# Kernel tuning notes

Hardware: AMD Instinct MI355X
Metric: run time of the kernel (lower is better)

## Reference

```python
import jax, jax.numpy as jnp
import numpy as np

H = 128      # num_hidden
C = 384      # num_in
K = 32       # neighbors
N = 10000    # nodes
SCALE = 30.0
EPS = 1e-5

def _gelu(x):
    return jax.nn.gelu(x, approximate=False)  # torch GELU default is exact erf

def _ln(x, g, b):
    m = jnp.mean(x, axis=-1, keepdims=True)
    v = jnp.mean((x - m) ** 2, axis=-1, keepdims=True)
    return (x - m) * jax.lax.rsqrt(v + EPS) * g + b

def setup_inputs() -> dict:
    key = jax.random.key(0)
    ks = jax.random.split(key, 12)
    s = lambda fan_in: 1.0 / np.sqrt(fan_in)
    # weights stored [in, out] (transposed vs torch nn.Linear)
    return {
        "h_V": jax.random.normal(ks[0], (N, H), jnp.float32),
        "h_E": jax.random.normal(ks[1], (N, K, C), jnp.float32),
        "mask_V": jnp.ones((N,), jnp.float32),
        "mask_attend": jnp.ones((N, K), jnp.float32),
        "W1_w": jax.random.uniform(ks[2], (H + C, H), jnp.float32, -s(H + C), s(H + C)),
        "W1_b": jnp.zeros((H,), jnp.float32),
        "W2_w": jax.random.uniform(ks[3], (H, H), jnp.float32, -s(H), s(H)),
        "W2_b": jnp.zeros((H,), jnp.float32),
        "W3_w": jax.random.uniform(ks[4], (H, H), jnp.float32, -s(H), s(H)),
        "W3_b": jnp.zeros((H,), jnp.float32),
        "ln1_g": jnp.ones((H,), jnp.float32),
        "ln1_b": jnp.zeros((H,), jnp.float32),
        "Win_w": jax.random.uniform(ks[5], (H, 4 * H), jnp.float32, -s(H), s(H)),
        "Win_b": jnp.zeros((4 * H,), jnp.float32),
        "Wout_w": jax.random.uniform(ks[6], (4 * H, H), jnp.float32, -s(4 * H), s(4 * H)),
        "Wout_b": jnp.zeros((H,), jnp.float32),
        "ln2_g": jnp.ones((H,), jnp.float32),
        "ln2_b": jnp.zeros((H,), jnp.float32),
    }

def reference(h_V, h_E, mask_V, mask_attend,
              W1_w, W1_b, W2_w, W2_b, W3_w, W3_b,
              ln1_g, ln1_b, Win_w, Win_b, Wout_w, Wout_b, ln2_g, ln2_b):
    # expand node features along neighbor axis and concat with edge features
    h_V_expand = jnp.broadcast_to(h_V[:, None, :], (h_V.shape[0], h_E.shape[1], h_V.shape[1]))
    h_EV = jnp.concatenate([h_V_expand, h_E], axis=-1)          # [N, K, H+C]
    # per-edge 3-layer MLP message
    h = _gelu(h_EV @ W1_w + W1_b)                               # [N, K, H]
    h = _gelu(h @ W2_w + W2_b)
    h_message = h @ W3_w + W3_b
    h_message = mask_attend[..., None] * h_message
    dh = jnp.sum(h_message, axis=-2) / SCALE                    # [N, H]
    h_V = _ln(h_V + dh, ln1_g, ln1_b)
    # position-wise FFN
    dh = _gelu(h_V @ Win_w + Win_b) @ Wout_w + Wout_b
    h_V = _ln(h_V + dh, ln2_g, ln2_b)
    h_V = mask_V[:, None] * h_V
    return h_V
```

## Files before the change

kernel.cpp:

```cpp
#include <hip/hip_runtime.h>
#include <hip/hip_bf16.h>

#define NH 128
#define NC 384
#define NK 32

typedef __attribute__((ext_vector_type(8))) short short8v;
typedef __attribute__((ext_vector_type(4))) float f32x4;

#define MFMA16(a, b, c) __builtin_amdgcn_mfma_f32_16x16x32_bf16((a), (b), (c), 0, 0, 0)

__device__ __forceinline__ ushort f2bf(float x) {
  __hip_bfloat16 h = __float2bfloat16(x);
  ushort u;
  __builtin_memcpy(&u, &h, 2);
  return u;
}

__device__ __forceinline__ short8v ld8(const ushort* p) {
  return *reinterpret_cast<const short8v*>(p);
}
__device__ __forceinline__ void st8(ushort* p, short8v v) {
  *reinterpret_cast<short8v*>(p) = v;
}

__device__ __forceinline__ short8v pack8(float4 a, float4 b) {
  short8v v;
  v[0] = (short)f2bf(a.x); v[1] = (short)f2bf(a.y);
  v[2] = (short)f2bf(a.z); v[3] = (short)f2bf(a.w);
  v[4] = (short)f2bf(b.x); v[5] = (short)f2bf(b.y);
  v[6] = (short)f2bf(b.z); v[7] = (short)f2bf(b.w);
  return v;
}

__device__ __forceinline__ float gelu_f(float x) {
  float x2 = x * x;
  float m = __builtin_fmaf(0.07135481283f, x2, 1.595769122f);
  float e = __expf(-x * m);
  return x * __builtin_amdgcn_rcpf(1.0f + e);
}

__global__ __launch_bounds__(256) void pack_w(
    const float* __restrict__ W1, const float* __restrict__ W2,
    const float* __restrict__ W3, const float* __restrict__ Win,
    const float* __restrict__ Wout, ushort* __restrict__ ws) {
  int id = blockIdx.x * 256 + threadIdx.x;
  if (id < 65536) {
    int t = id, k = t >> 7, c = t & 127;
    ws[(((k >> 3) << 7) + c) * 8 + (k & 7)] = f2bf(W1[t]);
  } else if (id < 81920) {
    int t = id - 65536, k = t >> 7, c = t & 127;
    ws[65536 + (((k >> 3) << 7) + c) * 8 + (k & 7)] = f2bf(W2[t]);
  } else if (id < 98304) {
    int t = id - 81920, k = t >> 7, c = t & 127;
    ws[81920 + (((k >> 3) << 7) + c) * 8 + (k & 7)] = f2bf(W3[t]);
  } else if (id < 163840) {
    int t = id - 98304, k = t >> 9, c = t & 511;
    ws[98304 + (((k >> 3) << 9) + c) * 8 + (k & 7)] = f2bf(Win[t]);
  } else {
    int t = id - 163840, k = t >> 7, c = t & 127;
    ws[163840 + (((k >> 3) << 7) + c) * 8 + (k & 7)] = f2bf(Wout[t]);
  }
}

__global__ __launch_bounds__(512, 4) void msg_kernel(
    const float* __restrict__ hV, const float* __restrict__ hE,
    const float* __restrict__ mAtt, const ushort* __restrict__ wsu,
    const float* __restrict__ b1, const float* __restrict__ b2,
    const float* __restrict__ b3, const float* __restrict__ g1,
    const float* __restrict__ be1, float* __restrict__ hmidf,
    ushort* __restrict__ hmidb, int N) {
  const ushort* W1p = wsu;
  const ushort* W2p = wsu + 65536;
  const ushort* W3p = wsu + 81920;

  __shared__ ushort sEb[2][64 * 128];
  __shared__ ushort sHV[2 * NH];
  __shared__ ushort sH1[64 * 128];
  __shared__ float  sDh[2 * NH];
  __shared__ float  sRed[16];
  ushort* sH2 = sEb[0];

  const int tid = threadIdx.x;
  const int w = tid >> 6, lane = tid & 63;
  const int g = lane >> 4, lr = lane & 15;
  const int n0 = blockIdx.x * 2;

  const int row = tid >> 3, cb = tid & 7;
  const int node = row >> 5, e = row & 31;
  const bool valid = (n0 + node) < N;
  const float* src = hE + (valid ? ((size_t)(n0 + node) * NK + e) * NC : 0);
  float4 L[3][2][2];
#pragma unroll
  for (int q = 0; q < 3; ++q)
#pragma unroll
    for (int h = 0; h < 2; ++h) {
      const float4* p = reinterpret_cast<const float4*>(src + q * 128 + h * 64 + cb * 8);
      L[q][h][0] = p[0];
      L[q][h][1] = p[1];
    }

  if (tid < 32) {
    const int nd = tid >> 4, c8 = tid & 15;
    short8v v = {0, 0, 0, 0, 0, 0, 0, 0};
    if (n0 + nd < N) {
      const float4* p = reinterpret_cast<const float4*>(hV + (size_t)(n0 + nd) * NH + c8 * 8);
      v = pack8(p[0], p[1]);
    }
    st8(sHV + nd * NH + c8 * 8, v);
  }

  const int rsw = row & 15;
#pragma unroll
  for (int h = 0; h < 2; ++h) {
    short8v v = valid ? pack8(L[0][h][0], L[0][h][1]) : (short8v){0, 0, 0, 0, 0, 0, 0, 0};
    st8(&sEb[0][row * 128 + (((cb + 8 * h) ^ rsw) << 3)], v);
  }
  __syncthreads();

  const int colbase = (w << 4) + lr;
  f32x4 acc[4];
#pragma unroll
  for (int rt = 0; rt < 4; ++rt) acc[rt] = (f32x4){0.f, 0.f, 0.f, 0.f};

#pragma unroll
  for (int kt = 0; kt < 4; ++kt) {
    short8v b = ld8(W1p + ((kt * 4 + g) * 128 + colbase) * 8);
    short8v a0 = ld8(sHV + kt * 32 + g * 8);
    short8v a1 = ld8(sHV + NH + kt * 32 + g * 8);
    acc[0] = MFMA16(a0, b, acc[0]);
    acc[1] = MFMA16(a0, b, acc[1]);
    acc[2] = MFMA16(a1, b, acc[2]);
    acc[3] = MFMA16(a1, b, acc[3]);
  }
#pragma unroll
  for (int j = 0; j < 4; ++j) {
    short8v b = ld8(W1p + (((4 + j) * 4 + g) * 128 + colbase) * 8);
    const int kcg = j * 4 + g;
#pragma unroll
    for (int rt = 0; rt < 4; ++rt) {
      const int r2 = rt * 16 + lr;
      short8v a = ld8(&sEb[0][r2 * 128 + ((kcg ^ (r2 & 15)) << 3)]);
      acc[rt] = MFMA16(a, b, acc[rt]);
    }
  }
#pragma unroll
  for (int h = 0; h < 2; ++h) {
    short8v v = valid ? pack8(L[1][h][0], L[1][h][1]) : (short8v){0, 0, 0, 0, 0, 0, 0, 0};
    st8(&sEb[1][row * 128 + (((cb + 8 * h) ^ rsw) << 3)], v);
  }
  __syncthreads();

#pragma unroll
  for (int j = 0; j < 4; ++j) {
    short8v b = ld8(W1p + (((8 + j) * 4 + g) * 128 + colbase) * 8);
    const int kcg = j * 4 + g;
#pragma unroll
    for (int rt = 0; rt < 4; ++rt) {
      const int r2 = rt * 16 + lr;
      short8v a = ld8(&sEb[1][r2 * 128 + ((kcg ^ (r2 & 15)) << 3)]);
      acc[rt] = MFMA16(a, b, acc[rt]);
    }
  }
#pragma unroll
  for (int h = 0; h < 2; ++h) {
    short8v v = valid ? pack8(L[2][h][0], L[2][h][1]) : (short8v){0, 0, 0, 0, 0, 0, 0, 0};
    st8(&sEb[0][row * 128 + (((cb + 8 * h) ^ rsw) << 3)], v);
  }
  __syncthreads();

#pragma unroll
  for (int j = 0; j < 4; ++j) {
    short8v b = ld8(W1p + (((12 + j) * 4 + g) * 128 + colbase) * 8);
    const int kcg = j * 4 + g;
#pragma unroll
    for (int rt = 0; rt < 4; ++rt) {
      const int r2 = rt * 16 + lr;
      short8v a = ld8(&sEb[0][r2 * 128 + ((kcg ^ (r2 & 15)) << 3)]);
      acc[rt] = MFMA16(a, b, acc[rt]);
    }
  }
  {
    const float bias = b1[colbase];
#pragma unroll
    for (int rt = 0; rt < 4; ++rt) {
#pragma unroll
      for (int i = 0; i < 4; ++i) {
        const int rr = rt * 16 + g * 4 + i;
        const float vv = gelu_f(acc[rt][i] + bias);
        sH1[rr * 128 + ((((colbase >> 3) ^ (rr & 15)) << 3) | (colbase & 7))] = f2bf(vv);
      }
    }
  }
  __syncthreads();

#pragma unroll
  for (int rt = 0; rt < 4; ++rt) acc[rt] = (f32x4){0.f, 0.f, 0.f, 0.f};
#pragma unroll
  for (int kt = 0; kt < 4; ++kt) {
    short8v b = ld8(W2p + ((kt * 4 + g) * 128 + colbase) * 8);
    const int kcg = kt * 4 + g;
#pragma unroll
    for (int rt = 0; rt < 4; ++rt) {
      const int r2 = rt * 16 + lr;
      short8v a = ld8(&sH1[r2 * 128 + ((kcg ^ (r2 & 15)) << 3)]);
      acc[rt] = MFMA16(a, b, acc[rt]);
    }
  }
  {
    const float bias = b2[colbase];
#pragma unroll
    for (int rt = 0; rt < 4; ++rt) {
#pragma unroll
      for (int i = 0; i < 4; ++i) {
        const int rr = rt * 16 + g * 4 + i;
        const float vv = gelu_f(acc[rt][i] + bias);
        sH2[rr * 128 + ((((colbase >> 3) ^ (rr & 15)) << 3) | (colbase & 7))] = f2bf(vv);
      }
    }
  }
  __syncthreads();

#pragma unroll
  for (int rt = 0; rt < 4; ++rt) acc[rt] = (f32x4){0.f, 0.f, 0.f, 0.f};
#pragma unroll
  for (int kt = 0; kt < 4; ++kt) {
    short8v b = ld8(W3p + ((kt * 4 + g) * 128 + colbase) * 8);
    const int kcg = kt * 4 + g;
#pragma unroll
    for (int rt = 0; rt < 4; ++rt) {
      const int r2 = rt * 16 + lr;
      short8v a = ld8(&sH2[r2 * 128 + ((kcg ^ (r2 & 15)) << 3)]);
      acc[rt] = MFMA16(a, b, acc[rt]);
    }
  }
  {
    const float bias = b3[colbase];
    float ns0 = 0.f, ns1 = 0.f;
#pragma unroll
    for (int rt = 0; rt < 4; ++rt) {
      const int nd = rt >> 1;
      float s = 0.f;
#pragma unroll
      for (int i = 0; i < 4; ++i) {
        const int e2 = (rt & 1) * 16 + g * 4 + i;
        const float m = (n0 + nd < N) ? mAtt[(size_t)(n0 + nd) * NK + e2] : 0.f;
        s += (acc[rt][i] + bias) * m;
      }
      s += __shfl_xor(s, 16, 64);
      s += __shfl_xor(s, 32, 64);
      if (rt < 2) ns0 += s; else ns1 += s;
    }
    if (g == 0) { sDh[colbase] = ns0; sDh[NH + colbase] = ns1; }
  }
  __syncthreads();

  float x_ln = 0.f;
  if (tid < 256) {
    const int nd = tid >> 7, i = tid & 127;
    const int gn = n0 + nd;
    if (gn < N) x_ln = hV[(size_t)gn * NH + i] + sDh[nd * NH + i] * (1.f / 30.f);
    float s = x_ln, qv = x_ln * x_ln;
#pragma unroll
    for (int d = 1; d < 64; d <<= 1) {
      s += __shfl_xor(s, d, 64);
      qv += __shfl_xor(qv, d, 64);
    }
    if (lane == 0) { sRed[w * 2] = s; sRed[w * 2 + 1] = qv; }
  }
  __syncthreads();
  if (tid < 256) {
    const int nd = tid >> 7, i = tid & 127;
    const int gn = n0 + nd;
    if (gn < N) {
      const int wb = nd * 2;
      const float s = sRed[wb * 2] + sRed[wb * 2 + 2];
      const float qv = sRed[wb * 2 + 1] + sRed[wb * 2 + 3];
      const float mean = s * (1.f / 128.f);
      const float var = qv * (1.f / 128.f) - mean * mean;
      const float y = (x_ln - mean) * rsqrtf(var + 1e-5f) * g1[i] + be1[i];
      hmidf[(size_t)gn * NH + i] = y;
      hmidb[(size_t)gn * NH + i] = f2bf(y);
    }
  }
}

__global__ __launch_bounds__(256, 4) void ffn_kernel(
    const ushort* __restrict__ wsu, const float* __restrict__ binf,
    const float* __restrict__ boutf, const float* __restrict__ g2,
    const float* __restrict__ be2, const float* __restrict__ maskV,
    const float* __restrict__ hmidf, const ushort* __restrict__ hmidb,
    float* __restrict__ out, int N) {
  const ushort* Winp = wsu + 98304;
  const ushort* Woutp = wsu + 163840;

  __shared__ ushort sX[16 * 128];
  __shared__ ushort sHf[16 * 512];
  __shared__ float  sY[16 * 132];

  const int tid = threadIdx.x;
  const int w = tid >> 6, lane = tid & 63;
  const int g = lane >> 4, lr = lane & 15;
  const int n0 = blockIdx.x * 16;

  {
    const int rr = tid >> 4, c8 = tid & 15;
    const int n = n0 + rr;
    short8v v = {0, 0, 0, 0, 0, 0, 0, 0};
    if (n < N) v = ld8(hmidb + (size_t)n * NH + c8 * 8);
    st8(sX + rr * 128 + ((c8 ^ (rr & 15)) << 3), v);
  }
  __syncthreads();

#pragma unroll
  for (int ct8 = 0; ct8 < 8; ++ct8) {
    const int col = (w * 8 + ct8) * 16 + lr;
    f32x4 a0acc = (f32x4){0.f, 0.f, 0.f, 0.f};
#pragma unroll
    for (int kt = 0; kt < 4; ++kt) {
      short8v b = ld8(Winp + ((kt * 4 + g) * 512 + col) * 8);
      const int kcg = kt * 4 + g;
      const int r0 = lr;
      short8v a0 = ld8(sX + r0 * 128 + ((kcg ^ (r0 & 15)) << 3));
      a0acc = MFMA16(a0, b, a0acc);
    }
    const float bi = binf[col];
#pragma unroll
    for (int i = 0; i < 4; ++i) {
      const int rr = g * 4 + i;
      const float v0 = gelu_f(a0acc[i] + bi);
      sHf[rr * 512 + ((((col >> 3) ^ (rr & 15)) << 3) | (col & 7))] = f2bf(v0);
    }
  }
  __syncthreads();

  f32x4 o0 = (f32x4){0.f, 0.f, 0.f, 0.f}, o1 = o0;
#pragma unroll
  for (int kt = 0; kt < 16; ++kt) {
    const int kcg = kt * 4 + g;
    const int c0 = (2 * w) * 16 + lr, c1 = (2 * w + 1) * 16 + lr;
    short8v b0 = ld8(Woutp + (kcg * 128 + c0) * 8);
    short8v b1 = ld8(Woutp + (kcg * 128 + c1) * 8);
    const int r0 = lr;
    short8v a0 = ld8(sHf + r0 * 512 + ((kcg ^ (r0 & 15)) << 3));
    o0 = MFMA16(a0, b0, o0);
    o1 = MFMA16(a0, b1, o1);
  }
#pragma unroll
  for (int ct = 0; ct < 2; ++ct) {
    const int col = (2 * w + ct) * 16 + lr;
    const float bo = boutf[col];
    const f32x4 oo = ct ? o1 : o0;
#pragma unroll
    for (int i = 0; i < 4; ++i) {
      const int rr = g * 4 + i;
      const int n = n0 + rr;
      const float resid = (n < N) ? hmidf[(size_t)n * NH + col] : 0.f;
      sY[rr * 132 + col] = oo[i] + bo + resid;
    }
  }
  __syncthreads();

  {
    const int rr = tid >> 4, qq = tid & 15;
    const int n = n0 + rr;
    float vals[8];
    float s = 0.f, qs = 0.f;
    const float* yr = sY + rr * 132 + qq * 8;
#pragma unroll
    for (int j = 0; j < 8; ++j) { float x = yr[j]; vals[j] = x; s += x; qs += x * x; }
    s += __shfl_xor(s, 1, 64);  qs += __shfl_xor(qs, 1, 64);
    s += __shfl_xor(s, 2, 64);  qs += __shfl_xor(qs, 2, 64);
    s += __shfl_xor(s, 4, 64);  qs += __shfl_xor(qs, 4, 64);
    s += __shfl_xor(s, 8, 64);  qs += __shfl_xor(qs, 8, 64);
    const float mean = s * (1.f / 128.f);
    const float var = qs * (1.f / 128.f) - mean * mean;
    const float rs = rsqrtf(var + 1e-5f);
    if (n < N) {
      const float mv = maskV[n];
#pragma unroll
      for (int j = 0; j < 8; ++j) {
        const int col = qq * 8 + j;
        out[(size_t)n * NH + col] = ((vals[j] - mean) * rs * g2[col] + be2[col]) * mv;
      }
    }
  }
}

extern "C" void kernel_launch(void* const* d_in, const int* in_sizes, int n_in,
                              void* d_out, int out_size, void* d_ws, size_t ws_size,
                              hipStream_t stream) {
  const float* hV   = (const float*)d_in[0];
  const float* hE   = (const float*)d_in[1];
  const float* mV   = (const float*)d_in[2];
  const float* mAtt = (const float*)d_in[3];
  const float* W1   = (const float*)d_in[4];
  const float* b1   = (const float*)d_in[5];
  const float* W2   = (const float*)d_in[6];
  const float* b2   = (const float*)d_in[7];
  const float* W3   = (const float*)d_in[8];
  const float* b3   = (const float*)d_in[9];
  const float* g1   = (const float*)d_in[10];
  const float* be1  = (const float*)d_in[11];
  const float* Win  = (const float*)d_in[12];
  const float* binf = (const float*)d_in[13];
  const float* Wout = (const float*)d_in[14];
  const float* bout = (const float*)d_in[15];
  const float* g2   = (const float*)d_in[16];
  const float* be2  = (const float*)d_in[17];

  const int N = in_sizes[0] / NH;

  ushort* wsu = (ushort*)d_ws;
  float*  hmidf = (float*)((char*)d_ws + 458752);
  ushort* hmidb = (ushort*)((char*)d_ws + 458752 + (size_t)N * NH * 4);
  float*  outp = (float*)d_out;

  pack_w<<<896, 256, 0, stream>>>(W1, W2, W3, Win, Wout, wsu);
  msg_kernel<<<(N + 1) / 2, 512, 0, stream>>>(hV, hE, mAtt, wsu, b1, b2, b3,
                                              g1, be1, hmidf, hmidb, N);
  ffn_kernel<<<(N + 15) / 16, 256, 0, stream>>>(wsu, binf, bout, g2, be2, mV,
                                                hmidf, hmidb, outp, N);
  (void)n_in; (void)out_size; (void)ws_size;
}
```

Before: 183.0 us.

## Fuse message and FFN kernels into persistent kernel with software-pipelined edge loads

Merges the message MLP kernel and the FFN kernel into one persistent kernel with a fixed grid of 512 blocks. Each block loops over node pairs and prefetches the next pair's edge features, node features and masks into registers and double-buffered LDS while the current pair computes. The post-LN1 intermediate stays in shared memory (up to 20 rows), and the FFN plus LN2 run at the end on those rows, so the global hmid round trip and the second launch go away. The trade-off is fewer blocks (512 instead of 5000), more synchronisation per iteration and higher LDS/register pressure, which may cut occupancy and weaken latency hiding.

```diff
diff --git a/kernel.cpp b/kernel.cpp
--- a/kernel.cpp
+++ b/kernel.cpp
@@ -63,325 +63,341 @@
   }
 }
 
-__global__ __launch_bounds__(512, 4) void msg_kernel(
+__global__ __launch_bounds__(512, 4) void msg_ffn(
     const float* __restrict__ hV, const float* __restrict__ hE,
-    const float* __restrict__ mAtt, const ushort* __restrict__ wsu,
+    const float* __restrict__ maskV, const float* __restrict__ mAtt,
+    const ushort* __restrict__ wsu,
     const float* __restrict__ b1, const float* __restrict__ b2,
     const float* __restrict__ b3, const float* __restrict__ g1,
-    const float* __restrict__ be1, float* __restrict__ hmidf,
-    ushort* __restrict__ hmidb, int N) {
+    const float* __restrict__ be1, const float* __restrict__ binf,
+    const float* __restrict__ bout, const float* __restrict__ g2,
+    const float* __restrict__ be2, float* __restrict__ out, int N) {
   const ushort* W1p = wsu;
   const ushort* W2p = wsu + 65536;
   const ushort* W3p = wsu + 81920;
-
-  __shared__ ushort sEb[2][64 * 128];
-  __shared__ ushort sHV[2 * NH];
-  __shared__ ushort sH1[64 * 128];
-  __shared__ float  sDh[2 * NH];
+  const ushort* Winp = wsu + 98304;
+  const ushort* Woutp = wsu + 163840;
+
+  __shared__ ushort sEb[2][8192];
+  __shared__ float  sHmidF[20 * 132];
+  __shared__ ushort sHV[2][256];
+  __shared__ float  sHVf[2][256];
+  __shared__ float  sMA[2][64];
+  __shared__ float  sDh[256];
   __shared__ float  sRed[16];
-  ushort* sH2 = sEb[0];
 
   const int tid = threadIdx.x;
   const int w = tid >> 6, lane = tid & 63;
   const int g = lane >> 4, lr = lane & 15;
-  const int n0 = blockIdx.x * 2;
-
-  const int row = tid >> 3, cb = tid & 7;
-  const int node = row >> 5, e = row & 31;
-  const bool valid = (n0 + node) < N;
-  const float* src = hE + (valid ? ((size_t)(n0 + node) * NK + e) * NC : 0);
-  float4 L[3][2][2];
-#pragma unroll
-  for (int q = 0; q < 3; ++q)
+  const int colbase = (w << 4) + lr;
+
+  const int pairsTotal = (N + 1) >> 1;
+  const int bId = blockIdx.x;
+  const int stride = gridDim.x;
+  const int T = (bId < pairsTotal) ? ((pairsTotal - bId + stride - 1) / stride) : 0;
+
+  const int srow = tid >> 3, scb = tid & 7;
+  const int snode = srow >> 5, sedge = srow & 31;
+  const int rsw = srow & 15;
+
+  float4 Lb0[2][2], Lb1[2][2], Lc2[2][2];
+  float4 hvreg = (float4){0.f, 0.f, 0.f, 0.f};
+  float  mareg = 0.f;
+  bool   zhold = true;
+
+  auto hEbase = [&](int p) -> const float* {
+    int n = 2 * p + snode;
+    int nc = n < N ? n : 0;
+    return hE + ((size_t)nc * NK + sedge) * NC + scb * 8;
+  };
+  auto loadCh = [&](const float* bp, int q, float4 L[2][2]) {
+    const float4* p0 = reinterpret_cast<const float4*>(bp + q * 128);
+    const float4* p1 = reinterpret_cast<const float4*>(bp + q * 128 + 64);
+    L[0][0] = p0[0]; L[0][1] = p0[1];
+    L[1][0] = p1[0]; L[1][1] = p1[1];
+  };
+  auto writeCh = [&](ushort* buf, float4 L[2][2], bool zz) {
 #pragma unroll
     for (int h = 0; h < 2; ++h) {
-      const float4* p = reinterpret_cast<const float4*>(src + q * 128 + h * 64 + cb * 8);
-      L[q][h][0] = p[0];
-      L[q][h][1] = p[1];
-    }
-
-  if (tid < 32) {
-    const int nd = tid >> 4, c8 = tid & 15;
-    short8v v = {0, 0, 0, 0, 0, 0, 0, 0};
-    if (n0 + nd < N) {
-      const float4* p = reinterpret_cast<const float4*>(hV + (size_t)(n0 + nd) * NH + c8 * 8);
-      v = pack8(p[0], p[1]);
-    }
-    st8(sHV + nd * NH + c8 * 8, v);
-  }
-
-  const int rsw = row & 15;
-#pragma unroll
-  for (int h = 0; h < 2; ++h) {
-    short8v v = valid ? pack8(L[0][h][0], L[0][h][1]) : (short8v){0, 0, 0, 0, 0, 0, 0, 0};
-    st8(&sEb[0][row * 128 + (((cb + 8 * h) ^ rsw) << 3)], v);
-  }
-  __syncthreads();
-
-  const int colbase = (w << 4) + lr;
-  f32x4 acc[4];
-#pragma unroll
-  for (int rt = 0; rt < 4; ++rt) acc[rt] = (f32x4){0.f, 0.f, 0.f, 0.f};
-
-#pragma unroll
-  for (int kt = 0; kt < 4; ++kt) {
-    short8v b = ld8(W1p + ((kt * 4 + g) * 128 + colbase) * 8);
-    short8v a0 = ld8(sHV + kt * 32 + g * 8);
-    short8v a1 = ld8(sHV + NH + kt * 32 + g * 8);
-    acc[0] = MFMA16(a0, b, acc[0]);
-    acc[1] = MFMA16(a0, b, acc[1]);
-    acc[2] = MFMA16(a1, b, acc[2]);
-    acc[3] = MFMA16(a1, b, acc[3]);
-  }
-#pragma unroll
-  for (int j = 0; j < 4; ++j) {
-    short8v b = ld8(W1p + (((4 + j) * 4 + g) * 128 + colbase) * 8);
-    const int kcg = j * 4 + g;
-#pragma unroll
-    for (int rt = 0; rt < 4; ++rt) {
-      const int r2 = rt * 16 + lr;
-      short8v a = ld8(&sEb[0][r2 * 128 + ((kcg ^ (r2 & 15)) << 3)]);
-      acc[rt] = MFMA16(a, b, acc[rt]);
-    }
-  }
-#pragma unroll
-  for (int h = 0; h < 2; ++h) {
-    short8v v = valid ? pack8(L[1][h][0], L[1][h][1]) : (short8v){0, 0, 0, 0, 0, 0, 0, 0};
-    st8(&sEb[1][row * 128 + (((cb + 8 * h) ^ rsw) << 3)], v);
-  }
-  __syncthreads();
-
-#pragma unroll
-  for (int j = 0; j < 4; ++j) {
-    short8v b = ld8(W1p + (((8 + j) * 4 + g) * 128 + colbase) * 8);
-    const int kcg = j * 4 + g;
-#pragma unroll
-    for (int rt = 0; rt < 4; ++rt) {
-      const int r2 = rt * 16 + lr;
-      short8v a = ld8(&sEb[1][r2 * 128 + ((kcg ^ (r2 & 15)) << 3)]);
-      acc[rt] = MFMA16(a, b, acc[rt]);
-    }
-  }
-#pragma unroll
-  for (int h = 0; h < 2; ++h) {
-    short8v v = valid ? pack8(L[2][h][0], L[2][h][1]) : (short8v){0, 0, 0, 0, 0, 0, 0, 0};
-    st8(&sEb[0][row * 128 + (((cb + 8 * h) ^ rsw) << 3)], v);
-  }
-  __syncthreads();
-
-#pragma unroll
-  for (int j = 0; j < 4; ++j) {
-    short8v b = ld8(W1p + (((12 + j) * 4 + g) * 128 + colbase) * 8);
-    const int kcg = j * 4 + g;
-#pragma unroll
-    for (int rt = 0; rt < 4; ++rt) {
-      const int r2 = rt * 16 + lr;
-      short8v a = ld8(&sEb[0][r2 * 128 + ((kcg ^ (r2 & 15)) << 3)]);
-      acc[rt] = MFMA16(a, b, acc[rt]);
-    }
-  }
-  {
-    const float bias = b1[colbase];
-#pragma unroll
-    for (int rt = 0; rt < 4; ++rt) {
+      short8v v = zz ? (short8v){0, 0, 0, 0, 0, 0, 0, 0} : pack8(L[h][0], L[h][1]);
+      st8(buf + srow * 128 + (((scb + 8 * h) ^ rsw) << 3), v);
+    }
+  };
+  auto loadHVMA = [&](int p) {
+    if (tid < 64) {
+      int nd = tid >> 5, c4 = tid & 31;
+      int n = 2 * p + nd;
+      int nc = n < N ? n : 0;
+      hvreg = *reinterpret_cast<const float4*>(hV + (size_t)nc * NH + c4 * 4);
+      if (n >= N) hvreg = (float4){0.f, 0.f, 0.f, 0.f};
+      mareg = (n < N) ? mAtt[(size_t)(2 * p) * NK + tid] : 0.f;
+    }
+  };
+  auto storeHVMA = [&](int par) {
+    if (tid < 64) {
+      int nd = tid >> 5, c4 = tid & 31;
+      *reinterpret_cast<float4*>(&sHVf[par][nd * 128 + c4 * 4]) = hvreg;
+      ushort4 hb;
+      hb.x = f2bf(hvreg.x); hb.y = f2bf(hvreg.y);
+      hb.z = f2bf(hvreg.z); hb.w = f2bf(hvreg.w);
+      *reinterpret_cast<ushort4*>(&sHV[par][nd * 128 + c4 * 4]) = hb;
+      sMA[par][tid] = mareg;
+    }
+  };
+  auto mfmaChunk = [&](const ushort* buf, int ktBase, f32x4 acc[4]) {
+#pragma unroll
+    for (int j = 0; j < 4; ++j) {
+      short8v bfr = ld8(W1p + (((ktBase + j) * 4 + g) * 128 + colbase) * 8);
+      const int kcg = j * 4 + g;
+#pragma unroll
+      for (int rt = 0; rt < 4; ++rt) {
+        const int row = rt * 16 + lr;
+        short8v a = ld8(buf + row * 128 + ((kcg ^ (row & 15)) << 3));
+        acc[rt] = MFMA16(a, bfr, acc[rt]);
+      }
+    }
+  };
+  auto mfma128 = [&](const ushort* Wp, const ushort* buf, f32x4 acc[4]) {
+#pragma unroll
+    for (int kt = 0; kt < 4; ++kt) {
+      short8v bfr = ld8(Wp + ((kt * 4 + g) * 128 + colbase) * 8);
+      const int kcg = kt * 4 + g;
+#pragma unroll
+      for (int rt = 0; rt < 4; ++rt) {
+        const int row = rt * 16 + lr;
+        short8v a = ld8(buf + row * 128 + ((kcg ^ (row & 15)) << 3));
+        acc[rt] = MFMA16(a, bfr, acc[rt]);
+      }
+    }
+  };
+  auto epiStore = [&](ushort* buf, f32x4 acc[4], const float* bias) {
+    const float bs = bias[colbase];
+#pragma unroll
+    for (int rt = 0; rt < 4; ++rt)
 #pragma unroll
       for (int i = 0; i < 4; ++i) {
         const int rr = rt * 16 + g * 4 + i;
-        const float vv = gelu_f(acc[rt][i] + bias);
-        sH1[rr * 128 + ((((colbase >> 3) ^ (rr & 15)) << 3) | (colbase & 7))] = f2bf(vv);
-      }
-    }
+        buf[rr * 128 + ((((colbase >> 3) ^ (rr & 15)) << 3) | (colbase & 7))] =
+            f2bf(gelu_f(acc[rt][i] + bs));
+      }
+  };
+
+  if (T > 0) {
+    const float* bp = hEbase(bId);
+    const bool z0 = (2 * bId + snode) >= N;
+    loadCh(bp, 0, Lb0);
+    loadCh(bp, 1, Lb1);
+    loadCh(bp, 2, Lc2);
+    loadHVMA(bId);
+    writeCh(sEb[0], Lb0, z0);
+    writeCh(sEb[1], Lb1, z0);
+    zhold = z0;
+    storeHVMA(0);
+    __syncthreads();
   }
-  __syncthreads();
-
-#pragma unroll
-  for (int rt = 0; rt < 4; ++rt) acc[rt] = (f32x4){0.f, 0.f, 0.f, 0.f};
-#pragma unroll
-  for (int kt = 0; kt < 4; ++kt) {
-    short8v b = ld8(W2p + ((kt * 4 + g) * 128 + colbase) * 8);
-    const int kcg = kt * 4 + g;
-#pragma unroll
-    for (int rt = 0; rt < 4; ++rt) {
-      const int r2 = rt * 16 + lr;
-      short8v a = ld8(&sH1[r2 * 128 + ((kcg ^ (r2 & 15)) << 3)]);
-      acc[rt] = MFMA16(a, b, acc[rt]);
-    }
-  }
-  {
-    const float bias = b2[colbase];
-#pragma unroll
-    for (int rt = 0; rt < 4; ++rt) {
-#pragma unroll
-      for (int i = 0; i < 4; ++i) {
-        const int rr = rt * 16 + g * 4 + i;
-        const float vv = gelu_f(acc[rt][i] + bias);
-        sH2[rr * 128 + ((((colbase >> 3) ^ (rr & 15)) << 3) | (colbase & 7))] = f2bf(vv);
-      }
-    }
-  }
-  __syncthreads();
-
-#pragma unroll
-  for (int rt = 0; rt < 4; ++rt) acc[rt] = (f32x4){0.f, 0.f, 0.f, 0.f};
-#pragma unroll
-  for (int kt = 0; kt < 4; ++kt) {
-    short8v b = ld8(W3p + ((kt * 4 + g) * 128 + colbase) * 8);
-    const int kcg = kt * 4 + g;
-#pragma unroll
-    for (int rt = 0; rt < 4; ++rt) {
-      const int r2 = rt * 16 + lr;
-      short8v a = ld8(&sH2[r2 * 128 + ((kcg ^ (r2 & 15)) << 3)]);
-      acc[rt] = MFMA16(a, b, acc[rt]);
-    }
-  }
-  {
-    const float bias = b3[colbase];
-    float ns0 = 0.f, ns1 = 0.f;
-#pragma unroll
-    for (int rt = 0; rt < 4; ++rt) {
-      const int nd = rt >> 1;
-      float s = 0.f;
-#pragma unroll
-      for (int i = 0; i < 4; ++i) {
-        const int e2 = (rt & 1) * 16 + g * 4 + i;
-        const float m = (n0 + nd < N) ? mAtt[(size_t)(n0 + nd) * NK + e2] : 0.f;
-        s += (acc[rt][i] + bias) * m;
-      }
-      s += __shfl_xor(s, 16, 64);
-      s += __shfl_xor(s, 32, 64);
-      if (rt < 2) ns0 += s; else ns1 += s;
-    }
-    if (g == 0) { sDh[colbase] = ns0; sDh[NH + colbase] = ns1; }
-  }
-  __syncthreads();
-
-  float x_ln = 0.f;
-  if (tid < 256) {
-    const int nd = tid >> 7, i = tid & 127;
-    const int gn = n0 + nd;
-    if (gn < N) x_ln = hV[(size_t)gn * NH + i] + sDh[nd * NH + i] * (1.f / 30.f);
-    float s = x_ln, qv = x_ln * x_ln;
-#pragma unroll
-    for (int d = 1; d < 64; d <<= 1) {
-      s += __shfl_xor(s, d, 64);
-      qv += __shfl_xor(qv, d, 64);
-    }
-    if (lane == 0) { sRed[w * 2] = s; sRed[w * 2 + 1] = qv; }
-  }
-  __syncthreads();
-  if (tid < 256) {
-    const int nd = tid >> 7, i = tid & 127;
-    const int gn = n0 + nd;
-    if (gn < N) {
+
+  for (int t = 0; t < T; ++t) {
+    const int par = t & 1, nxt = par ^ 1;
+    ushort* bufX = sEb[par];
+    ushort* bufY = sEb[nxt];
+
+    const int pn = bId + (t + 1) * stride;
+    const int pc = pn < pairsTotal ? pn : 0;
+    const bool zb = (2 * pc + snode) >= N;
+    const float* bp = hEbase(pc);
+    loadCh(bp, 0, Lb0);
+    loadCh(bp, 1, Lb1);
+    loadHVMA(pc);
+
+    f32x4 acc[4];
+#pragma unroll
+    for (int rt = 0; rt < 4; ++rt) acc[rt] = (f32x4){0.f, 0.f, 0.f, 0.f};
+#pragma unroll
+    for (int kt = 0; kt < 4; ++kt) {
+      short8v bfr = ld8(W1p + ((kt * 4 + g) * 128 + colbase) * 8);
+      short8v a0 = ld8(&sHV[par][kt * 32 + g * 8]);
+      short8v a1 = ld8(&sHV[par][128 + kt * 32 + g * 8]);
+      acc[0] = MFMA16(a0, bfr, acc[0]);
+      acc[1] = MFMA16(a0, bfr, acc[1]);
+      acc[2] = MFMA16(a1, bfr, acc[2]);
+      acc[3] = MFMA16(a1, bfr, acc[3]);
+    }
+    mfmaChunk(bufX, 4, acc);
+    __syncthreads();
+    writeCh(bufX, Lc2, zhold);
+    loadCh(bp, 2, Lc2);
+    zhold = zb;
+    mfmaChunk(bufY, 8, acc);
+    __syncthreads();
+    mfmaChunk(bufX, 12, acc);
+    __syncthreads();
+    epiStore(bufY, acc, b1);
+    __syncthreads();
+
+    f32x4 acc2[4];
+#pragma unroll
+    for (int rt = 0; rt < 4; ++rt) acc2[rt] = (f32x4){0.f, 0.f, 0.f, 0.f};
+    mfma128(W2p, bufY, acc2);
+    epiStore(bufX, acc2, b2);
+    __syncthreads();
+
+    f32x4 acc3[4];
+#pragma unroll
+    for (int rt = 0; rt < 4; ++rt) acc3[rt] = (f32x4){0.f, 0.f, 0.f, 0.f};
+    mfma128(W3p, bufX, acc3);
+    writeCh(bufY, Lb0, zb);
+    {
+      const float bias = b3[colbase];
+      float ns0 = 0.f, ns1 = 0.f;
+#pragma unroll
+      for (int rt = 0; rt < 4; ++rt) {
+        float s = 0.f;
+#pragma unroll
+        for (int i = 0; i < 4; ++i) {
+          const int e2 = (rt & 1) * 16 + g * 4 + i;
+          const int nd = rt >> 1;
+          s += (acc3[rt][i] + bias) * sMA[par][nd * 32 + e2];
+        }
+        s += __shfl_xor(s, 16, 64);
+        s += __shfl_xor(s, 32, 64);
+        if (rt < 2) ns0 += s; else ns1 += s;
+      }
+      if (g == 0) { sDh[colbase] = ns0; sDh[128 + colbase] = ns1; }
+    }
+    __syncthreads();
+
+    float x_ln = 0.f;
+    if (tid < 256) {
+      const int nd = tid >> 7, i = tid & 127;
+      x_ln = sHVf[par][nd * 128 + i] + sDh[nd * 128 + i] * (1.f / 30.f);
+      float s = x_ln, qv = x_ln * x_ln;
+#pragma unroll
+      for (int d = 1; d < 64; d <<= 1) {
+        s += __shfl_xor(s, d, 64);
+        qv += __shfl_xor(qv, d, 64);
+      }
+      if (lane == 0) { sRed[w * 2] = s; sRed[w * 2 + 1] = qv; }
+    }
+    writeCh(bufX, Lb1, zb);
+    storeHVMA(nxt);
+    __syncthreads();
+    if (tid < 256) {
+      const int nd = tid >> 7, i = tid & 127;
       const int wb = nd * 2;
       const float s = sRed[wb * 2] + sRed[wb * 2 + 2];
       const float qv = sRed[wb * 2 + 1] + sRed[wb * 2 + 3];
       const float mean = s * (1.f / 128.f);
       const float var = qv * (1.f / 128.f) - mean * mean;
       const float y = (x_ln - mean) * rsqrtf(var + 1e-5f) * g1[i] + be1[i];
-      hmidf[(size_t)gn * NH + i] = y;
-      hmidb[(size_t)gn * NH + i] = f2bf(y);
-    }
+      sHmidF[(2 * t + nd) * 132 + i] = y;
+    }
+    __syncthreads();
   }
-}
-
-__global__ __launch_bounds__(256, 4) void ffn_kernel(
-    const ushort* __restrict__ wsu, const float* __restrict__ binf,
-    const float* __restrict__ boutf, const float* __restrict__ g2,
-    const float* __restrict__ be2, const float* __restrict__ maskV,
-    const float* __restrict__ hmidf, const ushort* __restrict__ hmidb,
-    float* __restrict__ out, int N) {
-  const ushort* Winp = wsu + 98304;
-  const ushort* Woutp = wsu + 163840;
-
-  __shared__ ushort sX[16 * 128];
-  __shared__ ushort sHf[16 * 512];
-  __shared__ float  sY[16 * 132];
-
-  const int tid = threadIdx.x;
-  const int w = tid >> 6, lane = tid & 63;
-  const int g = lane >> 4, lr = lane & 15;
-  const int n0 = blockIdx.x * 16;
-
-  {
-    const int rr = tid >> 4, c8 = tid & 15;
-    const int n = n0 + rr;
-    short8v v = {0, 0, 0, 0, 0, 0, 0, 0};
-    if (n < N) v = ld8(hmidb + (size_t)n * NH + c8 * 8);
-    st8(sX + rr * 128 + ((c8 ^ (rr & 15)) << 3), v);
-  }
-  __syncthreads();
-
-#pragma unroll
-  for (int ct8 = 0; ct8 < 8; ++ct8) {
-    const int col = (w * 8 + ct8) * 16 + lr;
-    f32x4 a0acc = (f32x4){0.f, 0.f, 0.f, 0.f};
+
+  if (T > 0) {
+    const int R = 2 * T;
+    ushort* sHf = &sEb[0][0];
+    float*  sYF = reinterpret_cast<float*>(
+        reinterpret_cast<char*>(&sEb[0][0]) + 20480);
+
+    f32x4 accI[4][2];
+#pragma unroll
+    for (int ct = 0; ct < 4; ++ct)
+#pragma unroll
+      for (int rt = 0; rt < 2; ++rt) accI[ct][rt] = (f32x4){0.f, 0.f, 0.f, 0.f};
 #pragma unroll
     for (int kt = 0; kt < 4; ++kt) {
-      short8v b = ld8(Winp + ((kt * 4 + g) * 512 + col) * 8);
+      short8v afr[2];
+#pragma unroll
+      for (int rt = 0; rt < 2; ++rt) {
+        const int row = rt * 16 + lr;
+        if (row < R) {
+          const float4* ap =
+              reinterpret_cast<const float4*>(&sHmidF[row * 132 + kt * 32 + g * 8]);
+          afr[rt] = pack8(ap[0], ap[1]);
+        } else {
+          afr[rt] = (short8v){0, 0, 0, 0, 0, 0, 0, 0};
+        }
+      }
+#pragma unroll
+      for (int ct = 0; ct < 4; ++ct) {
+        const int col = (w << 6) + ct * 16 + lr;
+        short8v bfr = ld8(Winp + ((kt * 4 + g) * 512 + col) * 8);
+        accI[ct][0] = MFMA16(afr[0], bfr, accI[ct][0]);
+        accI[ct][1] = MFMA16(afr[1], bfr, accI[ct][1]);
+      }
+    }
+    __syncthreads();
+#pragma unroll
+    for (int ct = 0; ct < 4; ++ct) {
+      const int col = (w << 6) + ct * 16 + lr;
+      const float bi = binf[col];
+      const int c8 = col >> 3;
+#pragma unroll
+      for (int rt = 0; rt < 2; ++rt)
+#pragma unroll
+        for (int i = 0; i < 4; ++i) {
+          const int row = rt * 16 + g * 4 + i;
+          if (row < R)
+            sHf[row * 512 + (((c8 & 48) | ((c8 ^ row) & 15)) << 3) + (col & 7)] =
+                f2bf(gelu_f(accI[ct][rt][i] + bi));
+        }
+    }
+    __syncthreads();
+
+    f32x4 accO[2];
+    accO[0] = (f32x4){0.f, 0.f, 0.f, 0.f};
+    accO[1] = accO[0];
+#pragma unroll
+    for (int kt = 0; kt < 16; ++kt) {
       const int kcg = kt * 4 + g;
-      const int r0 = lr;
-      short8v a0 = ld8(sX + r0 * 128 + ((kcg ^ (r0 & 15)) << 3));
-      a0acc = MFMA16(a0, b, a0acc);
-    }
-    const float bi = binf[col];
-#pragma unroll
-    for (int i = 0; i < 4; ++i) {
-      const int rr = g * 4 + i;
-      const float v0 = gelu_f(a0acc[i] + bi);
-      sHf[rr * 512 + ((((col >> 3) ^ (rr & 15)) << 3) | (col & 7))] = f2bf(v0);
-    }
-  }
-  __syncthreads();
-
-  f32x4 o0 = (f32x4){0.f, 0.f, 0.f, 0.f}, o1 = o0;
-#pragma unroll
-  for (int kt = 0; kt < 16; ++kt) {
-    const int kcg = kt * 4 + g;
-    const int c0 = (2 * w) * 16 + lr, c1 = (2 * w + 1) * 16 + lr;
-    short8v b0 = ld8(Woutp + (kcg * 128 + c0) * 8);
-    short8v b1 = ld8(Woutp + (kcg * 128 + c1) * 8);
-    const int r0 = lr;
-    short8v a0 = ld8(sHf + r0 * 512 + ((kcg ^ (r0 & 15)) << 3));
-    o0 = MFMA16(a0, b0, o0);
-    o1 = MFMA16(a0, b1, o1);
-  }
-#pragma unroll
-  for (int ct = 0; ct < 2; ++ct) {
-    const int col = (2 * w + ct) * 16 + lr;
-    const float bo = boutf[col];
-    const f32x4 oo = ct ? o1 : o0;
-#pragma unroll
-    for (int i = 0; i < 4; ++i) {
-      const int rr = g * 4 + i;
-      const int n = n0 + rr;
-      const float resid = (n < N) ? hmidf[(size_t)n * NH + col] : 0.f;
-      sY[rr * 132 + col] = oo[i] + bo + resid;
-    }
-  }
-  __syncthreads();
-
-  {
-    const int rr = tid >> 4, qq = tid & 15;
-    const int n = n0 + rr;
-    float vals[8];
-    float s = 0.f, qs = 0.f;
-    const float* yr = sY + rr * 132 + qq * 8;
-#pragma unroll
-    for (int j = 0; j < 8; ++j) { float x = yr[j]; vals[j] = x; s += x; qs += x * x; }
-    s += __shfl_xor(s, 1, 64);  qs += __shfl_xor(qs, 1, 64);
-    s += __shfl_xor(s, 2, 64);  qs += __shfl_xor(qs, 2, 64);
-    s += __shfl_xor(s, 4, 64);  qs += __shfl_xor(qs, 4, 64);
-    s += __shfl_xor(s, 8, 64);  qs += __shfl_xor(qs, 8, 64);
-    const float mean = s * (1.f / 128.f);
-    const float var = qs * (1.f / 128.f) - mean * mean;
-    const float rs = rsqrtf(var + 1e-5f);
-    if (n < N) {
-      const float mv = maskV[n];
-#pragma unroll
-      for (int j = 0; j < 8; ++j) {
-        const int col = qq * 8 + j;
-        out[(size_t)n * NH + col] = ((vals[j] - mean) * rs * g2[col] + be2[col]) * mv;
+      short8v bfr = ld8(Woutp + (kcg * 128 + colbase) * 8);
+#pragma unroll
+      for (int rt = 0; rt < 2; ++rt) {
+        const int row = rt * 16 + lr;
+        short8v a = (row < R)
+            ? ld8(sHf + row * 512 + (((kcg & 48) | ((kcg ^ row) & 15)) << 3))
+            : (short8v){0, 0, 0, 0, 0, 0, 0, 0};
+        accO[rt] = MFMA16(a, bfr, accO[rt]);
+      }
+    }
+    {
+      const float bo = bout[colbase];
+#pragma unroll
+      for (int rt = 0; rt < 2; ++rt)
+#pragma unroll
+        for (int i = 0; i < 4; ++i) {
+          const int row = rt * 16 + g * 4 + i;
+          if (row < R)
+            sYF[row * 132 + colbase] =
+                accO[rt][i] + bo + sHmidF[row * 132 + colbase];
+        }
+    }
+    __syncthreads();
+
+    if (tid < R * 16) {
+      const int row = tid >> 4, qq = tid & 15;
+      const float* yr = sYF + row * 132 + qq * 8;
+      float vals[8];
+      float s = 0.f, qs = 0.f;
+#pragma unroll
+      for (int j = 0; j < 8; ++j) { float x = yr[j]; vals[j] = x; s += x; qs += x * x; }
+      s += __shfl_xor(s, 1, 64);  qs += __shfl_xor(qs, 1, 64);
+      s += __shfl_xor(s, 2, 64);  qs += __shfl_xor(qs, 2, 64);
+      s += __shfl_xor(s, 4, 64);  qs += __shfl_xor(qs, 4, 64);
+      s += __shfl_xor(s, 8, 64);  qs += __shfl_xor(qs, 8, 64);
+      const float mean = s * (1.f / 128.f);
+      const float var = qs * (1.f / 128.f) - mean * mean;
+      const float rs = rsqrtf(var + 1e-5f);
+      const int n = 2 * (bId + (row >> 1) * stride) + (row & 1);
+      if (n < N) {
+        const float mv = maskV[n];
+#pragma unroll
+        for (int j = 0; j < 8; ++j) {
+          const int col = qq * 8 + j;
+          out[(size_t)n * NH + col] =
+              ((vals[j] - mean) * rs * g2[col] + be2[col]) * mv;
+        }
       }
     }
   }
@@ -412,14 +428,15 @@
   const int N = in_sizes[0] / NH;
 
   ushort* wsu = (ushort*)d_ws;
-  float*  hmidf = (float*)((char*)d_ws + 458752);
-  ushort* hmidb = (ushort*)((char*)d_ws + 458752 + (size_t)N * NH * 4);
-  float*  outp = (float*)d_out;
 
   pack_w<<<896, 256, 0, stream>>>(W1, W2, W3, Win, Wout, wsu);
-  msg_kernel<<<(N + 1) / 2, 512, 0, stream>>>(hV, hE, mAtt, wsu, b1, b2, b3,
-                                              g1, be1, hmidf, hmidb, N);
-  ffn_kernel<<<(N + 15) / 16, 256, 0, stream>>>(wsu, binf, bout, g2, be2, mV,
-                                                hmidf, hmidb, outp, N);
+
+  const int pairs = (N + 1) / 2;
+  int grid = 512;
+  if ((pairs + grid - 1) / grid > 10)
+    grid = (pairs + 9) / 10;
+
+  msg_ffn<<<grid, 512, 0, stream>>>(hV, hE, mV, mAtt, wsu, b1, b2, b3, g1,
+                                    be1, binf, bout, g2, be2, (float*)d_out, N);
   (void)n_in; (void)out_size; (void)ws_size;
 }
```

New measurement: 442.8 us. 142% more time.

## Make message kernel persistent with cross-iteration prefetch of edge features

Applied to the files above, without the earlier changes.

Replaces the one-block-per-node-pair message kernel with a persistent kernel on a grid capped at 512 blocks that loops over node pairs. It prefetches the next pair's h_E chunks and h_V into registers while the current pair's MLP runs, aiming to hide global-load latency behind MFMA work and cut block launch overhead. Shared buffers are reused across stages. The cost is more barriers, higher register pressure, and possibly lower occupancy, since 512 blocks may not fill 256 CUs at 4 blocks each.

```diff
diff --git a/kernel.cpp b/kernel.cpp
--- a/kernel.cpp
+++ b/kernel.cpp
@@ -63,7 +63,63 @@
   }
 }
 
-__global__ __launch_bounds__(512, 4) void msg_kernel(
+
+__device__ __forceinline__ void load_chunk(const float* __restrict__ hE,
+    int pr, int chunk, int snode, int sedge, int scb, int N,
+    float4& L0, float4& L1, float4& L2, float4& L3) {
+  int n = 2 * pr + snode;
+  int nc = n < N ? n : 0;
+  const float* base = hE + ((size_t)nc * NK + sedge) * NC + chunk * 128;
+  const float4* p0 = reinterpret_cast<const float4*>(base + scb * 8);
+  const float4* p1 = reinterpret_cast<const float4*>(base + 64 + scb * 8);
+  L0 = p0[0]; L1 = p0[1]; L2 = p1[0]; L3 = p1[1];
+}
+
+__device__ __forceinline__ void write_chunk(ushort* __restrict__ buf,
+    float4 L0, float4 L1, float4 L2, float4 L3,
+    int srow, int scb, int rsw, bool zz) {
+  short8v v0, v1;
+  if (zz) {
+    v0 = (short8v){0, 0, 0, 0, 0, 0, 0, 0};
+    v1 = v0;
+  } else {
+    v0 = pack8(L0, L1);
+    v1 = pack8(L2, L3);
+  }
+  st8(buf + srow * 128 + ((scb ^ rsw) << 3), v0);
+  st8(buf + srow * 128 + (((scb + 8) ^ rsw) << 3), v1);
+}
+
+__device__ __forceinline__ void mfma_chunk(const ushort* __restrict__ buf,
+    const ushort* __restrict__ Wp, int ktBase, f32x4 acc[4],
+    int g, int lr, int colbase) {
+#pragma unroll
+  for (int j = 0; j < 4; ++j) {
+    short8v b = ld8(Wp + (((ktBase + j) * 4 + g) * 128 + colbase) * 8);
+    const int kcg = j * 4 + g;
+#pragma unroll
+    for (int rt = 0; rt < 4; ++rt) {
+      const int row = rt * 16 + lr;
+      short8v a = ld8(buf + row * 128 + ((kcg ^ (row & 15)) << 3));
+      acc[rt] = MFMA16(a, b, acc[rt]);
+    }
+  }
+}
+
+__device__ __forceinline__ void epi_store(ushort* __restrict__ buf,
+    const f32x4 acc[4], const float* __restrict__ bias, int colbase, int g) {
+  const float bs = bias[colbase];
+#pragma unroll
+  for (int rt = 0; rt < 4; ++rt)
+#pragma unroll
+    for (int i = 0; i < 4; ++i) {
+      const int rr = rt * 16 + g * 4 + i;
+      buf[rr * 128 + ((((colbase >> 3) ^ (rr & 15)) << 3) | (colbase & 7))] =
+          f2bf(gelu_f(acc[rt][i] + bs));
+    }
+}
+
+__global__ __launch_bounds__(512, 4) void msg_pers(
     const float* __restrict__ hV, const float* __restrict__ hE,
     const float* __restrict__ mAtt, const ushort* __restrict__ wsu,
     const float* __restrict__ b1, const float* __restrict__ b2,
@@ -74,214 +130,154 @@
   const ushort* W2p = wsu + 65536;
   const ushort* W3p = wsu + 81920;
 
-  __shared__ ushort sEb[2][64 * 128];
-  __shared__ ushort sHV[2 * NH];
-  __shared__ ushort sH1[64 * 128];
-  __shared__ float  sDh[2 * NH];
+  __shared__ ushort sA[8192];
+  __shared__ ushort sB[8192];
+  __shared__ ushort sHV[256];
+  __shared__ float  sDh[256];
   __shared__ float  sRed[16];
-  ushort* sH2 = sEb[0];
 
   const int tid = threadIdx.x;
   const int w = tid >> 6, lane = tid & 63;
   const int g = lane >> 4, lr = lane & 15;
-  const int n0 = blockIdx.x * 2;
-
-  const int row = tid >> 3, cb = tid & 7;
-  const int node = row >> 5, e = row & 31;
-  const bool valid = (n0 + node) < N;
-  const float* src = hE + (valid ? ((size_t)(n0 + node) * NK + e) * NC : 0);
-  float4 L[3][2][2];
-#pragma unroll
-  for (int q = 0; q < 3; ++q)
-#pragma unroll
-    for (int h = 0; h < 2; ++h) {
-      const float4* p = reinterpret_cast<const float4*>(src + q * 128 + h * 64 + cb * 8);
-      L[q][h][0] = p[0];
-      L[q][h][1] = p[1];
-    }
-
+  const int colbase = (w << 4) + lr;
+
+  const int srow = tid >> 3, scb = tid & 7;
+  const int snode = srow >> 5, sedge = srow & 31;
+  const int rsw = srow & 15;
+
+  const int pairs = (N + 1) >> 1;
+  const int stride = gridDim.x;
+  const int bId = blockIdx.x;
+  const int T = (pairs - bId + stride - 1) / stride;
+
+  float4 rA0, rA1, rA2, rA3, rB0, rB1, rB2, rB3;
+  float4 hv0 = (float4){0.f, 0.f, 0.f, 0.f}, hv1 = hv0;
+
+  load_chunk(hE, bId, 0, snode, sedge, scb, N, rA0, rA1, rA2, rA3);
+  load_chunk(hE, bId, 1, snode, sedge, scb, N, rB0, rB1, rB2, rB3);
   if (tid < 32) {
     const int nd = tid >> 4, c8 = tid & 15;
-    short8v v = {0, 0, 0, 0, 0, 0, 0, 0};
-    if (n0 + nd < N) {
-      const float4* p = reinterpret_cast<const float4*>(hV + (size_t)(n0 + nd) * NH + c8 * 8);
-      v = pack8(p[0], p[1]);
-    }
-    st8(sHV + nd * NH + c8 * 8, v);
-  }
-
-  const int rsw = row & 15;
-#pragma unroll
-  for (int h = 0; h < 2; ++h) {
-    short8v v = valid ? pack8(L[0][h][0], L[0][h][1]) : (short8v){0, 0, 0, 0, 0, 0, 0, 0};
-    st8(&sEb[0][row * 128 + (((cb + 8 * h) ^ rsw) << 3)], v);
-  }
-  __syncthreads();
-
-  const int colbase = (w << 4) + lr;
-  f32x4 acc[4];
-#pragma unroll
-  for (int rt = 0; rt < 4; ++rt) acc[rt] = (f32x4){0.f, 0.f, 0.f, 0.f};
-
-#pragma unroll
-  for (int kt = 0; kt < 4; ++kt) {
-    short8v b = ld8(W1p + ((kt * 4 + g) * 128 + colbase) * 8);
-    short8v a0 = ld8(sHV + kt * 32 + g * 8);
-    short8v a1 = ld8(sHV + NH + kt * 32 + g * 8);
-    acc[0] = MFMA16(a0, b, acc[0]);
-    acc[1] = MFMA16(a0, b, acc[1]);
-    acc[2] = MFMA16(a1, b, acc[2]);
-    acc[3] = MFMA16(a1, b, acc[3]);
-  }
-#pragma unroll
-  for (int j = 0; j < 4; ++j) {
-    short8v b = ld8(W1p + (((4 + j) * 4 + g) * 128 + colbase) * 8);
-    const int kcg = j * 4 + g;
-#pragma unroll
-    for (int rt = 0; rt < 4; ++rt) {
-      const int r2 = rt * 16 + lr;
-      short8v a = ld8(&sEb[0][r2 * 128 + ((kcg ^ (r2 & 15)) << 3)]);
-      acc[rt] = MFMA16(a, b, acc[rt]);
-    }
-  }
-#pragma unroll
-  for (int h = 0; h < 2; ++h) {
-    short8v v = valid ? pack8(L[1][h][0], L[1][h][1]) : (short8v){0, 0, 0, 0, 0, 0, 0, 0};
-    st8(&sEb[1][row * 128 + (((cb + 8 * h) ^ rsw) << 3)], v);
-  }
-  __syncthreads();
-
-#pragma unroll
-  for (int j = 0; j < 4; ++j) {
-    short8v b = ld8(W1p + (((8 + j) * 4 + g) * 128 + colbase) * 8);
-    const int kcg = j * 4 + g;
-#pragma unroll
-    for (int rt = 0; rt < 4; ++rt) {
-      const int r2 = rt * 16 + lr;
-      short8v a = ld8(&sEb[1][r2 * 128 + ((kcg ^ (r2 & 15)) << 3)]);
-      acc[rt] = MFMA16(a, b, acc[rt]);
-    }
-  }
-#pragma unroll
-  for (int h = 0; h < 2; ++h) {
-    short8v v = valid ? pack8(L[2][h][0], L[2][h][1]) : (short8v){0, 0, 0, 0, 0, 0, 0, 0};
-    st8(&sEb[0][row * 128 + (((cb + 8 * h) ^ rsw) << 3)], v);
-  }
-  __syncthreads();
-
-#pragma unroll
-  for (int j = 0; j < 4; ++j) {
-    short8v b = ld8(W1p + (((12 + j) * 4 + g) * 128 + colbase) * 8);
-    const int kcg = j * 4 + g;
-#pragma unroll
-    for (int rt = 0; rt < 4; ++rt) {
-      const int r2 = rt * 16 + lr;
-      short8v a = ld8(&sEb[0][r2 * 128 + ((kcg ^ (r2 & 15)) << 3)]);
-      acc[rt] = MFMA16(a, b, acc[rt]);
-    }
-  }
-  {
-    const float bias = b1[colbase];
-#pragma unroll
-    for (int rt = 0; rt < 4; ++rt) {
-#pragma unroll
-      for (int i = 0; i < 4; ++i) {
-        const int rr = rt * 16 + g * 4 + i;
-        const float vv = gelu_f(acc[rt][i] + bias);
-        sH1[rr * 128 + ((((colbase >> 3) ^ (rr & 15)) << 3) | (colbase & 7))] = f2bf(vv);
+    const int n = 2 * bId + nd;
+    const int ncl = n < N ? n : 0;
+    const float4* hp = reinterpret_cast<const float4*>(hV + (size_t)ncl * NH + c8 * 8);
+    float4 h0 = hp[0], h1 = hp[1];
+    if (n >= N) { h0 = (float4){0.f, 0.f, 0.f, 0.f}; h1 = h0; }
+    st8(sHV + nd * 128 + c8 * 8, pack8(h0, h1));
+  }
+
+  for (int t = 0; t < T; ++t) {
+    const int p = bId + t * stride;
+    const bool zz = (2 * p + snode) >= N;
+
+    write_chunk(sA, rA0, rA1, rA2, rA3, srow, scb, rsw, zz);
+    write_chunk(sB, rB0, rB1, rB2, rB3, srow, scb, rsw, zz);
+    __syncthreads();
+
+    float4 rC0, rC1, rC2, rC3;
+    load_chunk(hE, p, 2, snode, sedge, scb, N, rC0, rC1, rC2, rC3);
+    f32x4 acc[4];
+#pragma unroll
+    for (int rt = 0; rt < 4; ++rt) acc[rt] = (f32x4){0.f, 0.f, 0.f, 0.f};
+#pragma unroll
+    for (int kt = 0; kt < 4; ++kt) {
+      short8v bfr = ld8(W1p + ((kt * 4 + g) * 128 + colbase) * 8);
+      short8v a0 = ld8(sHV + kt * 32 + g * 8);
+      short8v a1 = ld8(sHV + 128 + kt * 32 + g * 8);
+      acc[0] = MFMA16(a0, bfr, acc[0]);
+      acc[1] = MFMA16(a0, bfr, acc[1]);
+      acc[2] = MFMA16(a1, bfr, acc[2]);
+      acc[3] = MFMA16(a1, bfr, acc[3]);
+    }
+    mfma_chunk(sA, W1p, 4, acc, g, lr, colbase);
+    __syncthreads();
+
+    mfma_chunk(sB, W1p, 8, acc, g, lr, colbase);
+    write_chunk(sA, rC0, rC1, rC2, rC3, srow, scb, rsw, zz);
+    __syncthreads();
+
+    mfma_chunk(sA, W1p, 12, acc, g, lr, colbase);
+    epi_store(sB, acc, b1, colbase, g);
+    __syncthreads();
+
+    const int pn = bId + (t + 1) * stride;
+    const int pnc = pn < pairs ? pn : bId;
+    load_chunk(hE, pnc, 0, snode, sedge, scb, N, rA0, rA1, rA2, rA3);
+    f32x4 acc2[4];
+#pragma unroll
+    for (int rt = 0; rt < 4; ++rt) acc2[rt] = (f32x4){0.f, 0.f, 0.f, 0.f};
+    mfma_chunk(sB, W2p, 0, acc2, g, lr, colbase);
+    epi_store(sA, acc2, b2, colbase, g);
+    __syncthreads();
+
+    load_chunk(hE, pnc, 1, snode, sedge, scb, N, rB0, rB1, rB2, rB3);
+    if (tid < 32) {
+      const int nd = tid >> 4, c8 = tid & 15;
+      const int n = 2 * pnc + nd;
+      const int ncl = n < N ? n : 0;
+      const float4* hp = reinterpret_cast<const float4*>(hV + (size_t)ncl * NH + c8 * 8);
+      hv0 = hp[0]; hv1 = hp[1];
+      if (n >= N) { hv0 = (float4){0.f, 0.f, 0.f, 0.f}; hv1 = hv0; }
+    }
+    f32x4 acc3[4];
+#pragma unroll
+    for (int rt = 0; rt < 4; ++rt) acc3[rt] = (f32x4){0.f, 0.f, 0.f, 0.f};
+    mfma_chunk(sA, W3p, 0, acc3, g, lr, colbase);
+    {
+      const float bias = b3[colbase];
+      float ns0 = 0.f, ns1 = 0.f;
+#pragma unroll
+      for (int rt = 0; rt < 4; ++rt) {
+        const int nd = rt >> 1;
+        float s = 0.f;
+#pragma unroll
+        for (int i = 0; i < 4; ++i) {
+          const int e2 = (rt & 1) * 16 + g * 4 + i;
+          const float m =
+              (2 * p + nd < N) ? mAtt[(size_t)(2 * p + nd) * NK + e2] : 0.f;
+          s += (acc3[rt][i] + bias) * m;
+        }
+        s += __shfl_xor(s, 16, 64);
+        s += __shfl_xor(s, 32, 64);
+        if (rt < 2) ns0 += s; else ns1 += s;
       }
-    }
-  }
-  __syncthreads();
-
-#pragma unroll
-  for (int rt = 0; rt < 4; ++rt) acc[rt] = (f32x4){0.f, 0.f, 0.f, 0.f};
-#pragma unroll
-  for (int kt = 0; kt < 4; ++kt) {
-    short8v b = ld8(W2p + ((kt * 4 + g) * 128 + colbase) * 8);
-    const int kcg = kt * 4 + g;
-#pragma unroll
-    for (int rt = 0; rt < 4; ++rt) {
-      const int r2 = rt * 16 + lr;
-      short8v a = ld8(&sH1[r2 * 128 + ((kcg ^ (r2 & 15)) << 3)]);
-      acc[rt] = MFMA16(a, b, acc[rt]);
-    }
-  }
-  {
-    const float bias = b2[colbase];
-#pragma unroll
-    for (int rt = 0; rt < 4; ++rt) {
-#pragma unroll
-      for (int i = 0; i < 4; ++i) {
-        const int rr = rt * 16 + g * 4 + i;
-        const float vv = gelu_f(acc[rt][i] + bias);
-        sH2[rr * 128 + ((((colbase >> 3) ^ (rr & 15)) << 3) | (colbase & 7))] = f2bf(vv);
+      if (g == 0) { sDh[colbase] = ns0; sDh[128 + colbase] = ns1; }
+    }
+    __syncthreads();
+
+    float x_ln = 0.f;
+    if (tid < 256) {
+      const int nd = tid >> 7, i = tid & 127;
+      const int gn = 2 * p + nd;
+      if (gn < N)
+        x_ln = hV[(size_t)gn * NH + i] + sDh[nd * NH + i] * (1.f / 30.f);
+      float s = x_ln, qv = x_ln * x_ln;
+#pragma unroll
+      for (int d = 1; d < 64; d <<= 1) {
+        s += __shfl_xor(s, d, 64);
+        qv += __shfl_xor(qv, d, 64);
       }
-    }
-  }
-  __syncthreads();
-
-#pragma unroll
-  for (int rt = 0; rt < 4; ++rt) acc[rt] = (f32x4){0.f, 0.f, 0.f, 0.f};
-#pragma unroll
-  for (int kt = 0; kt < 4; ++kt) {
-    short8v b = ld8(W3p + ((kt * 4 + g) * 128 + colbase) * 8);
-    const int kcg = kt * 4 + g;
-#pragma unroll
-    for (int rt = 0; rt < 4; ++rt) {
-      const int r2 = rt * 16 + lr;
-      short8v a = ld8(&sH2[r2 * 128 + ((kcg ^ (r2 & 15)) << 3)]);
-      acc[rt] = MFMA16(a, b, acc[rt]);
-    }
-  }
-  {
-    const float bias = b3[colbase];
-    float ns0 = 0.f, ns1 = 0.f;
-#pragma unroll
-    for (int rt = 0; rt < 4; ++rt) {
-      const int nd = rt >> 1;
-      float s = 0.f;
-#pragma unroll
-      for (int i = 0; i < 4; ++i) {
-        const int e2 = (rt & 1) * 16 + g * 4 + i;
-        const float m = (n0 + nd < N) ? mAtt[(size_t)(n0 + nd) * NK + e2] : 0.f;
-        s += (acc[rt][i] + bias) * m;
+      if (lane == 0) { sRed[w * 2] = s; sRed[w * 2 + 1] = qv; }
+    }
+    if (tid < 32) {
+      const int nd = tid >> 4, c8 = tid & 15;
+      st8(sHV + nd * 128 + c8 * 8, pack8(hv0, hv1));
+    }
+    __syncthreads();
+    if (tid < 256) {
+      const int nd = tid >> 7, i = tid & 127;
+      const int gn = 2 * p + nd;
+      if (gn < N) {
+        const int wb = nd * 2;
+        const float s = sRed[wb * 2] + sRed[wb * 2 + 2];
+        const float qv = sRed[wb * 2 + 1] + sRed[wb * 2 + 3];
+        const float mean = s * (1.f / 128.f);
+        const float var = qv * (1.f / 128.f) - mean * mean;
+        const float y = (x_ln - mean) * rsqrtf(var + 1e-5f) * g1[i] + be1[i];
+        hmidf[(size_t)gn * NH + i] = y;
+        hmidb[(size_t)gn * NH + i] = f2bf(y);
       }
-      s += __shfl_xor(s, 16, 64);
-      s += __shfl_xor(s, 32, 64);
-      if (rt < 2) ns0 += s; else ns1 += s;
-    }
-    if (g == 0) { sDh[colbase] = ns0; sDh[NH + colbase] = ns1; }
-  }
-  __syncthreads();
-
-  float x_ln = 0.f;
-  if (tid < 256) {
-    const int nd = tid >> 7, i = tid & 127;
-    const int gn = n0 + nd;
-    if (gn < N) x_ln = hV[(size_t)gn * NH + i] + sDh[nd * NH + i] * (1.f / 30.f);
-    float s = x_ln, qv = x_ln * x_ln;
-#pragma unroll
-    for (int d = 1; d < 64; d <<= 1) {
-      s += __shfl_xor(s, d, 64);
-      qv += __shfl_xor(qv, d, 64);
-    }
-    if (lane == 0) { sRed[w * 2] = s; sRed[w * 2 + 1] = qv; }
-  }
-  __syncthreads();
-  if (tid < 256) {
-    const int nd = tid >> 7, i = tid & 127;
-    const int gn = n0 + nd;
-    if (gn < N) {
-      const int wb = nd * 2;
-      const float s = sRed[wb * 2] + sRed[wb * 2 + 2];
-      const float qv = sRed[wb * 2 + 1] + sRed[wb * 2 + 3];
-      const float mean = s * (1.f / 128.f);
-      const float var = qv * (1.f / 128.f) - mean * mean;
-      const float y = (x_ln - mean) * rsqrtf(var + 1e-5f) * g1[i] + be1[i];
-      hmidf[(size_t)gn * NH + i] = y;
-      hmidb[(size_t)gn * NH + i] = f2bf(y);
-    }
+    }
+    __syncthreads();
   }
 }
 
@@ -414,12 +410,14 @@
   ushort* wsu = (ushort*)d_ws;
   float*  hmidf = (float*)((char*)d_ws + 458752);
   ushort* hmidb = (ushort*)((char*)d_ws + 458752 + (size_t)N * NH * 4);
-  float*  outp = (float*)d_out;
 
   pack_w<<<896, 256, 0, stream>>>(W1, W2, W3, Win, Wout, wsu);
-  msg_kernel<<<(N + 1) / 2, 512, 0, stream>>>(hV, hE, mAtt, wsu, b1, b2, b3,
-                                              g1, be1, hmidf, hmidb, N);
+
+  const int pairs = (N + 1) / 2;
+  const int grid = pairs < 512 ? pairs : 512;
+  msg_pers<<<grid, 512, 0, stream>>>(hV, hE, mAtt, wsu, b1, b2, b3, g1, be1,
+                                     hmidf, hmidb, N);
   ffn_kernel<<<(N + 15) / 16, 256, 0, stream>>>(wsu, binf, bout, g2, be2, mV,
-                                                hmidf, hmidb, outp, N);
+                                                hmidf, hmidb, (float*)d_out, N);
   (void)n_in; (void)out_size; (void)ws_size;
 }
```

Measured after the change: 336.8 us. 84.1% more time.
